# Kernel tuning notes

Hardware: AMD Instinct MI355X
Metric: run time of the kernel (lower is better)

The kernel has to match this reference:

```python
import jax, jax.numpy as jnp
import numpy as np

SIMS = 16
AMP = 1.0  # cfg['attention_amplifier']


def setup_inputs() -> dict:
    key = jax.random.key(0)
    k1, k2, k3 = jax.random.split(key, 3)
    B, F = 32, 2048
    data = jax.random.normal(k1, (B * SIMS, F), dtype=jnp.float32)
    attention = jax.random.normal(k2, (B * SIMS, F), dtype=jnp.float32)
    W = jax.random.normal(k3, (SIMS, 2 * SIMS), dtype=jnp.float32) * (1.0 / np.sqrt(2 * SIMS))
    b = jnp.zeros((SIMS,), dtype=jnp.float32)
    return {"data": data, "attention": attention, "W": W, "b": b}


def reference(data, attention, W, b):
    s = SIMS
    B = data.shape[0] // s
    inputs = data.reshape(B, s, -1)            # [B, s, F]
    attn_in = attention.reshape(B, s, -1)      # [B, s, G]
    # bmm(inputs^T, attention) -> [B, F, G]
    a = jnp.einsum('bsf,bsg->bfg', inputs, attn_in)
    a = jax.nn.log_softmax(a, axis=1)          # log_softmax over F dim (dim=1)
    # bmm(a, attention^T) -> [B, F, s]
    a = jnp.einsum('bfg,bsg->bfs', a, attn_in)
    concat = jnp.concatenate([jnp.swapaxes(a, 1, 2), inputs], axis=1)  # [B, 2s, F]
    concat = jnp.swapaxes(concat, 1, 2).reshape(-1, 2 * s)             # [B*F, 2s]
    gate = jax.nn.sigmoid(concat @ W.T + b)    # [B*F, s]
    # output.t().contiguous().view(data.shape): [s, B*F] row-major -> [B*s, F]
    gate = gate.T.reshape(data.shape)
    return gate * data * AMP
```

## Files before the change

### kernel.cpp

```cpp
#include <hip/hip_runtime.h>
#include <math.h>

#define LOG2E 1.44269504088896340736f
#define LN2   0.69314718055994530942f

typedef _Float16 half8 __attribute__((ext_vector_type(8)));
typedef float f32x4v __attribute__((ext_vector_type(4)));

#define AROW 24

template <bool ATOMIC>
__global__ __launch_bounds__(256, 4) void kA(const float* __restrict__ data,
                                             const float* __restrict__ attn,
                                             float* __restrict__ Lout) {
    __shared__ _Float16 AhB[128 * AROW];
    __shared__ _Float16 AlB[128 * AROW];
    const int tid = threadIdx.x;
    const int b = blockIdx.z, fb = blockIdx.y, gb = blockIdx.x;
    const int wave = tid >> 6, lane = tid & 63;
    const int n = lane & 15, q = lane >> 4;
    const int s0 = (q & 1) * 8;

    const float* Tb = attn + (size_t)b * 16 * 2048;
    half8 B1[2], B2[2];
#pragma unroll
    for (int ct = 0; ct < 2; ++ct) {
        const int g = gb * 128 + wave * 32 + ct * 16 + n;
        half8 bh, bl;
#pragma unroll
        for (int j = 0; j < 8; ++j) {
            float x = Tb[(size_t)(s0 + j) * 2048 + g] * LOG2E;
            _Float16 h = (_Float16)x;
            _Float16 l = (_Float16)(x - (float)h);
            bh[j] = h;
            bl[j] = (q < 2) ? l : (_Float16)0.0f;
        }
        B1[ct] = bh;
        B2[ct] = bl;
    }

    f32x4v cs0 = {0.f, 0.f, 0.f, 0.f}, cs1 = {0.f, 0.f, 0.f, 0.f};

    const float* Ab = data + (size_t)b * 16 * 2048 + fb * 1024;
    const int fst = tid >> 1;
    const int sh  = (tid & 1) * 8;
    const _Float16* aptr = ((q < 2) ? AhB : AlB) + n * AROW + s0;

    for (int chunk = 0; chunk < 8; ++chunk) {
        const float* Ac = Ab + chunk * 128;
        _Float16 hb[8], lb[8];
#pragma unroll
        for (int j = 0; j < 8; ++j) {
            float x = Ac[(size_t)(sh + j) * 2048 + fst];
            _Float16 h = (_Float16)x;
            hb[j] = h;
            lb[j] = (_Float16)(x - (float)h);
        }
        __syncthreads();
        half8 hv, lv;
#pragma unroll
        for (int j = 0; j < 8; ++j) { hv[j] = hb[j]; lv[j] = lb[j]; }
        *(half8*)(AhB + fst * AROW + sh) = hv;
        *(half8*)(AlB + fst * AROW + sh) = lv;
        __syncthreads();

#pragma unroll
        for (int rt = 0; rt < 8; ++rt) {
            half8 af = *(const half8*)(aptr + rt * 16 * AROW);
            f32x4v C = {0.f, 0.f, 0.f, 0.f};
            C = __builtin_amdgcn_mfma_f32_16x16x32_f16(af, B1[0], C, 0, 0, 0);
            C = __builtin_amdgcn_mfma_f32_16x16x32_f16(af, B2[0], C, 0, 0, 0);
            cs0[0] += __builtin_amdgcn_exp2f(C[0]);
            cs0[1] += __builtin_amdgcn_exp2f(C[1]);
            cs0[2] += __builtin_amdgcn_exp2f(C[2]);
            cs0[3] += __builtin_amdgcn_exp2f(C[3]);
            f32x4v D = {0.f, 0.f, 0.f, 0.f};
            D = __builtin_amdgcn_mfma_f32_16x16x32_f16(af, B1[1], D, 0, 0, 0);
            D = __builtin_amdgcn_mfma_f32_16x16x32_f16(af, B2[1], D, 0, 0, 0);
            cs1[0] += __builtin_amdgcn_exp2f(D[0]);
            cs1[1] += __builtin_amdgcn_exp2f(D[1]);
            cs1[2] += __builtin_amdgcn_exp2f(D[2]);
            cs1[3] += __builtin_amdgcn_exp2f(D[3]);
        }
    }

    float v0 = cs0[0] + cs0[1] + cs0[2] + cs0[3];
    float v1 = cs1[0] + cs1[1] + cs1[2] + cs1[3];
    v0 += __shfl_xor(v0, 16);
    v0 += __shfl_xor(v0, 32);
    v1 += __shfl_xor(v1, 16);
    v1 += __shfl_xor(v1, 32);
    if (q == 0) {
        const int g = gb * 128 + wave * 32 + n;
        if (ATOMIC) {
            atomicAdd(&Lout[(size_t)b * 2048 + g], v0);
            atomicAdd(&Lout[(size_t)b * 2048 + g + 16], v1);
        } else {
            Lout[((size_t)fb * 32 + b) * 2048 + g] = v0;
            Lout[((size_t)fb * 32 + b) * 2048 + g + 16] = v1;
        }
    }
}

#define TPAD 516
__global__ __launch_bounds__(256) void kTail(const float* __restrict__ attn,
                                             const float* __restrict__ Lpart, int nparts,
                                             float* __restrict__ Mpart,
                                             float* __restrict__ cpart) {
    __shared__ float Tsh[16 * TPAD];
    __shared__ float Lsh[512];
    __shared__ float red[16][17];
    const int tid = threadIdx.x;
    const int seg = blockIdx.x, b = blockIdx.y;
    const int g0 = seg * 512;

#pragma unroll
    for (int k = 0; k < 32; ++k) {
        int e = k * 256 + tid;
        int s = e >> 9, g = e & 511;
        Tsh[s * TPAD + g] = attn[(size_t)(b * 16 + s) * 2048 + g0 + g];
    }
#pragma unroll
    for (int k = 0; k < 2; ++k) {
        int g = k * 256 + tid;
        float sum = 0.f;
        for (int p = 0; p < nparts; ++p)
            sum += Lpart[((size_t)p * 32 + b) * 2048 + g0 + g];
        Lsh[g] = LN2 * __builtin_amdgcn_logf(sum);
    }
    __syncthreads();

    {
        const int t = tid & 15, i = tid >> 4;
        float acc = 0.f;
#pragma unroll
        for (int k = 0; k < 8; ++k) {
            float4 l  = *(const float4*)(Lsh + i * 32 + k * 4);
            float4 tv = *(const float4*)(Tsh + t * TPAD + i * 32 + k * 4);
            acc += l.x * tv.x + l.y * tv.y + l.z * tv.z + l.w * tv.w;
        }
        red[t][i] = acc;
    }
    __syncthreads();
    if (tid < 16) {
        float s = 0.f;
#pragma unroll
        for (int k = 0; k < 16; ++k) s += red[tid][k];
        cpart[((size_t)seg * 32 + b) * 16 + tid] = s;
    }

    {
        const int s = tid >> 4, t = tid & 15;
        float acc = 0.f;
#pragma unroll 4
        for (int qk = 0; qk < 128; ++qk) {
            float4 x = *(const float4*)(Tsh + s * TPAD + qk * 4);
            float4 y = *(const float4*)(Tsh + t * TPAD + qk * 4);
            acc += x.x * y.x + x.y * y.y + x.z * y.z + x.w * y.w;
        }
        Mpart[((size_t)seg * 32 + b) * 256 + tid] = acc;
    }
}

__global__ __launch_bounds__(256) void kFold(const float* __restrict__ Mpart,
                                             const float* __restrict__ cpart,
                                             const float* __restrict__ W,
                                             const float* __restrict__ bias,
                                             float* __restrict__ V,
                                             float* __restrict__ w0eff) {
    __shared__ float Msh[256];
    __shared__ float cl[16];
    const int b = blockIdx.x, tid = threadIdx.x;
    float m = 0.f;
#pragma unroll
    for (int p = 0; p < 4; ++p) m += Mpart[((size_t)p * 32 + b) * 256 + tid];
    Msh[tid] = m;
    if (tid < 16) {
        float c = 0.f;
#pragma unroll
        for (int p = 0; p < 4; ++p) c += cpart[((size_t)p * 32 + b) * 16 + tid];
        cl[tid] = c;
    }
    __syncthreads();
    const int s = tid >> 4, j = tid & 15;
    float acc = 0.f;
#pragma unroll
    for (int t = 0; t < 16; ++t) acc += Msh[s * 16 + t] * W[j * 32 + t];
    V[(size_t)b * 256 + s * 16 + j] = acc + W[j * 32 + 16 + s];
    if (s == 0) {
        float w0 = 0.f;
#pragma unroll
        for (int t = 0; t < 16; ++t) w0 += cl[t] * W[j * 32 + t];
        w0eff[b * 16 + j] = bias[j] - w0;
    }
}

__global__ __launch_bounds__(256) void kC(const float* __restrict__ data,
                                          const float* __restrict__ V,
                                          const float* __restrict__ w0eff,
                                          float* __restrict__ out) {
    const int tid = threadIdx.x;
    const int b = blockIdx.y;
    const int f = blockIdx.x * 256 + tid;
    float As[16];
#pragma unroll
    for (int s = 0; s < 16; ++s)
        As[s] = data[(size_t)(b * 16 + s) * 2048 + f];
    const float* Vb = V + (size_t)b * 256;
    const float* w0 = w0eff + b * 16;
#pragma unroll
    for (int j = 0; j < 16; ++j) {
        float p = w0[j];
#pragma unroll
        for (int s = 0; s < 16; ++s) p += As[s] * Vb[s * 16 + j];
        float e = __builtin_amdgcn_exp2f(-LOG2E * p);
        float gate = __builtin_amdgcn_rcpf(1.0f + e);
        size_t r = (size_t)(j * 32 + b) * 2048 + f;
        out[r] = gate * data[r];
    }
}

extern "C" void kernel_launch(void* const* d_in, const int* in_sizes, int n_in,
                              void* d_out, int out_size, void* d_ws, size_t ws_size,
                              hipStream_t stream) {
    const float* data = (const float*)d_in[0];
    const float* attn = (const float*)d_in[1];
    const float* W    = (const float*)d_in[2];
    const float* bias = (const float*)d_in[3];
    float* out = (float*)d_out;
    float* ws  = (float*)d_ws;

    const size_t LP = 2 * 32 * 2048;
    const size_t need_big = LP + 32768 + 2048 + 8192 + 512;

    if (ws_size >= need_big * sizeof(float)) {
        float* Lpart = ws;
        float* Mpart = ws + LP;
        float* cpart = Mpart + 32768;
        float* V     = cpart + 2048;
        float* w0eff = V + 8192;
        kA<false><<<dim3(16, 2, 32), 256, 0, stream>>>(data, attn, Lpart);
        kTail<<<dim3(4, 32), 256, 0, stream>>>(attn, Lpart, 2, Mpart, cpart);
        kFold<<<dim3(32), 256, 0, stream>>>(Mpart, cpart, W, bias, V, w0eff);
        kC<<<dim3(8, 32), 256, 0, stream>>>(data, V, w0eff, out);
    } else {
        float* Lsum  = ws;
        float* Mpart = ws + 65536;
        float* cpart = Mpart + 32768;
        float* V     = cpart + 2048;
        float* w0eff = V + 8192;
        hipMemsetAsync(Lsum, 0, 65536 * sizeof(float), stream);
        kA<true><<<dim3(16, 2, 32), 256, 0, stream>>>(data, attn, Lsum);
        kTail<<<dim3(4, 32), 256, 0, stream>>>(attn, Lsum, 1, Mpart, cpart);
        kFold<<<dim3(32), 256, 0, stream>>>(Mpart, cpart, W, bias, V, w0eff);
        kC<<<dim3(8, 32), 256, 0, stream>>>(data, V, w0eff, out);
    }
}
```

Before: 111.8 us.

## Fuse fold kernel into gating kernel and double split-F parallelism in kA/kTail

Removes the separate kFold launch: each kC2 block now reduces Mpart/cpart and computes V and w0 into shared memory before gating, cutting one kernel launch and a global round trip at the cost of redundant per-block fold work. kA splits F into 4 parts instead of 2, giving twice as many blocks with half the chunks each, and its load mapping now coalesces along f. kTail uses 8 segments of 256 instead of 4 of 512 to raise block count and uses two accumulators in the Gram loop. The partial-sum buffers grow accordingly.

```diff
diff --git a/kernel.cpp b/kernel.cpp
--- a/kernel.cpp
+++ b/kernel.cpp
@@ -41,12 +41,12 @@
 
     f32x4v cs0 = {0.f, 0.f, 0.f, 0.f}, cs1 = {0.f, 0.f, 0.f, 0.f};
 
-    const float* Ab = data + (size_t)b * 16 * 2048 + fb * 1024;
-    const int fst = tid >> 1;
-    const int sh  = (tid & 1) * 8;
+    const float* Ab = data + (size_t)b * 16 * 2048 + fb * 512;
+    const int fst = tid & 127;
+    const int sh  = (tid >> 7) * 8;
     const _Float16* aptr = ((q < 2) ? AhB : AlB) + n * AROW + s0;
 
-    for (int chunk = 0; chunk < 8; ++chunk) {
+    for (int chunk = 0; chunk < 4; ++chunk) {
         const float* Ac = Ab + chunk * 128;
         _Float16 hb[8], lb[8];
 #pragma unroll
@@ -102,31 +102,26 @@
     }
 }
 
-#define TPAD 516
+#define TP 260
 __global__ __launch_bounds__(256) void kTail(const float* __restrict__ attn,
                                              const float* __restrict__ Lpart, int nparts,
                                              float* __restrict__ Mpart,
                                              float* __restrict__ cpart) {
-    __shared__ float Tsh[16 * TPAD];
-    __shared__ float Lsh[512];
+    __shared__ float Tsh[16 * TP];
+    __shared__ float Lsh[256];
     __shared__ float red[16][17];
     const int tid = threadIdx.x;
     const int seg = blockIdx.x, b = blockIdx.y;
-    const int g0 = seg * 512;
-
-#pragma unroll
-    for (int k = 0; k < 32; ++k) {
-        int e = k * 256 + tid;
-        int s = e >> 9, g = e & 511;
-        Tsh[s * TPAD + g] = attn[(size_t)(b * 16 + s) * 2048 + g0 + g];
-    }
-#pragma unroll
-    for (int k = 0; k < 2; ++k) {
-        int g = k * 256 + tid;
+    const int g0 = seg * 256;
+
+#pragma unroll
+    for (int s = 0; s < 16; ++s)
+        Tsh[s * TP + tid] = attn[(size_t)(b * 16 + s) * 2048 + g0 + tid];
+    {
         float sum = 0.f;
         for (int p = 0; p < nparts; ++p)
-            sum += Lpart[((size_t)p * 32 + b) * 2048 + g0 + g];
-        Lsh[g] = LN2 * __builtin_amdgcn_logf(sum);
+            sum += Lpart[((size_t)p * 32 + b) * 2048 + g0 + tid];
+        Lsh[tid] = LN2 * __builtin_amdgcn_logf(sum);
     }
     __syncthreads();
 
@@ -134,9 +129,9 @@
         const int t = tid & 15, i = tid >> 4;
         float acc = 0.f;
 #pragma unroll
-        for (int k = 0; k < 8; ++k) {
-            float4 l  = *(const float4*)(Lsh + i * 32 + k * 4);
-            float4 tv = *(const float4*)(Tsh + t * TPAD + i * 32 + k * 4);
+        for (int k = 0; k < 4; ++k) {
+            float4 l  = *(const float4*)(Lsh + i * 16 + k * 4);
+            float4 tv = *(const float4*)(Tsh + t * TP + i * 16 + k * 4);
             acc += l.x * tv.x + l.y * tv.y + l.z * tv.z + l.w * tv.w;
         }
         red[t][i] = acc;
@@ -151,68 +146,71 @@
 
     {
         const int s = tid >> 4, t = tid & 15;
-        float acc = 0.f;
+        float a0 = 0.f, a1 = 0.f;
 #pragma unroll 4
-        for (int qk = 0; qk < 128; ++qk) {
-            float4 x = *(const float4*)(Tsh + s * TPAD + qk * 4);
-            float4 y = *(const float4*)(Tsh + t * TPAD + qk * 4);
-            acc += x.x * y.x + x.y * y.y + x.z * y.z + x.w * y.w;
-        }
-        Mpart[((size_t)seg * 32 + b) * 256 + tid] = acc;
-    }
-}
-
-__global__ __launch_bounds__(256) void kFold(const float* __restrict__ Mpart,
-                                             const float* __restrict__ cpart,
-                                             const float* __restrict__ W,
-                                             const float* __restrict__ bias,
-                                             float* __restrict__ V,
-                                             float* __restrict__ w0eff) {
+        for (int qk = 0; qk < 32; ++qk) {
+            float4 x = *(const float4*)(Tsh + s * TP + qk * 8);
+            float4 y = *(const float4*)(Tsh + t * TP + qk * 8);
+            a0 += x.x * y.x + x.y * y.y + x.z * y.z + x.w * y.w;
+            float4 x2 = *(const float4*)(Tsh + s * TP + qk * 8 + 4);
+            float4 y2 = *(const float4*)(Tsh + t * TP + qk * 8 + 4);
+            a1 += x2.x * y2.x + x2.y * y2.y + x2.z * y2.z + x2.w * y2.w;
+        }
+        Mpart[((size_t)seg * 32 + b) * 256 + tid] = a0 + a1;
+    }
+}
+
+__global__ __launch_bounds__(256) void kC2(const float* __restrict__ data,
+                                           const float* __restrict__ Mpart,
+                                           const float* __restrict__ cpart,
+                                           const float* __restrict__ W,
+                                           const float* __restrict__ bias,
+                                           float* __restrict__ out) {
     __shared__ float Msh[256];
-    __shared__ float cl[16];
-    const int b = blockIdx.x, tid = threadIdx.x;
-    float m = 0.f;
-#pragma unroll
-    for (int p = 0; p < 4; ++p) m += Mpart[((size_t)p * 32 + b) * 256 + tid];
-    Msh[tid] = m;
-    if (tid < 16) {
-        float c = 0.f;
-#pragma unroll
-        for (int p = 0; p < 4; ++p) c += cpart[((size_t)p * 32 + b) * 16 + tid];
-        cl[tid] = c;
-    }
-    __syncthreads();
-    const int s = tid >> 4, j = tid & 15;
-    float acc = 0.f;
-#pragma unroll
-    for (int t = 0; t < 16; ++t) acc += Msh[s * 16 + t] * W[j * 32 + t];
-    V[(size_t)b * 256 + s * 16 + j] = acc + W[j * 32 + 16 + s];
-    if (s == 0) {
-        float w0 = 0.f;
-#pragma unroll
-        for (int t = 0; t < 16; ++t) w0 += cl[t] * W[j * 32 + t];
-        w0eff[b * 16 + j] = bias[j] - w0;
-    }
-}
-
-__global__ __launch_bounds__(256) void kC(const float* __restrict__ data,
-                                          const float* __restrict__ V,
-                                          const float* __restrict__ w0eff,
-                                          float* __restrict__ out) {
+    __shared__ float csh[16];
+    __shared__ float Vsh[256];
+    __shared__ float w0sh[16];
     const int tid = threadIdx.x;
     const int b = blockIdx.y;
     const int f = blockIdx.x * 256 + tid;
+
+    {
+        float m = 0.f;
+#pragma unroll
+        for (int p = 0; p < 8; ++p) m += Mpart[((size_t)p * 32 + b) * 256 + tid];
+        Msh[tid] = m;
+        if (tid < 16) {
+            float c = 0.f;
+#pragma unroll
+            for (int p = 0; p < 8; ++p) c += cpart[((size_t)p * 32 + b) * 16 + tid];
+            csh[tid] = c;
+        }
+    }
+    __syncthreads();
+    {
+        const int s = tid >> 4, j = tid & 15;
+        float acc = 0.f;
+#pragma unroll
+        for (int t = 0; t < 16; ++t) acc += Msh[s * 16 + t] * W[j * 32 + t];
+        Vsh[s * 16 + j] = acc + W[j * 32 + 16 + s];
+        if (s == 0) {
+            float w0 = 0.f;
+#pragma unroll
+            for (int t = 0; t < 16; ++t) w0 += csh[t] * W[j * 32 + t];
+            w0sh[j] = bias[j] - w0;
+        }
+    }
+    __syncthreads();
+
     float As[16];
 #pragma unroll
     for (int s = 0; s < 16; ++s)
         As[s] = data[(size_t)(b * 16 + s) * 2048 + f];
-    const float* Vb = V + (size_t)b * 256;
-    const float* w0 = w0eff + b * 16;
 #pragma unroll
     for (int j = 0; j < 16; ++j) {
-        float p = w0[j];
-#pragma unroll
-        for (int s = 0; s < 16; ++s) p += As[s] * Vb[s * 16 + j];
+        float p = w0sh[j];
+#pragma unroll
+        for (int s = 0; s < 16; ++s) p += As[s] * Vsh[s * 16 + j];
         float e = __builtin_amdgcn_exp2f(-LOG2E * p);
         float gate = __builtin_amdgcn_rcpf(1.0f + e);
         size_t r = (size_t)(j * 32 + b) * 2048 + f;
@@ -230,29 +228,23 @@
     float* out = (float*)d_out;
     float* ws  = (float*)d_ws;
 
-    const size_t LP = 2 * 32 * 2048;
-    const size_t need_big = LP + 32768 + 2048 + 8192 + 512;
+    const size_t LP = 4 * 32 * 2048;
+    const size_t need_big = LP + 65536 + 4096;
 
     if (ws_size >= need_big * sizeof(float)) {
         float* Lpart = ws;
         float* Mpart = ws + LP;
-        float* cpart = Mpart + 32768;
-        float* V     = cpart + 2048;
-        float* w0eff = V + 8192;
-        kA<false><<<dim3(16, 2, 32), 256, 0, stream>>>(data, attn, Lpart);
-        kTail<<<dim3(4, 32), 256, 0, stream>>>(attn, Lpart, 2, Mpart, cpart);
-        kFold<<<dim3(32), 256, 0, stream>>>(Mpart, cpart, W, bias, V, w0eff);
-        kC<<<dim3(8, 32), 256, 0, stream>>>(data, V, w0eff, out);
+        float* cpart = Mpart + 65536;
+        kA<false><<<dim3(16, 4, 32), 256, 0, stream>>>(data, attn, Lpart);
+        kTail<<<dim3(8, 32), 256, 0, stream>>>(attn, Lpart, 4, Mpart, cpart);
+        kC2<<<dim3(8, 32), 256, 0, stream>>>(data, Mpart, cpart, W, bias, out);
     } else {
         float* Lsum  = ws;
         float* Mpart = ws + 65536;
-        float* cpart = Mpart + 32768;
-        float* V     = cpart + 2048;
-        float* w0eff = V + 8192;
+        float* cpart = Mpart + 65536;
         hipMemsetAsync(Lsum, 0, 65536 * sizeof(float), stream);
-        kA<true><<<dim3(16, 2, 32), 256, 0, stream>>>(data, attn, Lsum);
-        kTail<<<dim3(4, 32), 256, 0, stream>>>(attn, Lsum, 1, Mpart, cpart);
-        kFold<<<dim3(32), 256, 0, stream>>>(Mpart, cpart, W, bias, V, w0eff);
-        kC<<<dim3(8, 32), 256, 0, stream>>>(data, V, w0eff, out);
-    }
-}
+        kA<true><<<dim3(16, 4, 32), 256, 0, stream>>>(data, attn, Lsum);
+        kTail<<<dim3(8, 32), 256, 0, stream>>>(attn, Lsum, 1, Mpart, cpart);
+        kC2<<<dim3(8, 32), 256, 0, stream>>>(data, Mpart, cpart, W, bias, out);
+    }
+}
```

After: 94.99 us. 15.0% less time.
